# Kernel tuning notes

Measured on AMD Instinct MI355X. Metric: run time of the kernel, lower is better.

Reference implementation:

```python
import jax, jax.numpy as jnp
import numpy as np

PATCH = 3  # patch_size

def _extract_patches(feat):
    # feat: (c, h, w) -> (n_patches, c*9), patches in row-major spatial order
    c, h, w = feat.shape
    p = jax.lax.conv_general_dilated_patches(feat[None], (PATCH, PATCH), (1, 1), 'VALID')
    return p[0].reshape(c * PATCH * PATCH, -1).T  # (n, c*9)

def _match_single(feat_in, feat_ref):
    # faithful to feature_match_index(is_norm=True, norm_input=True)
    c, h, w = feat_in.shape
    def pxnorm(f):
        # F.normalize over channel dim per pixel (eps=1e-12)
        v = f.reshape(c, -1)
        n = jnp.sqrt(jnp.sum(v * v, axis=0, keepdims=True))
        return (v / jnp.maximum(n, 1e-12)).reshape(c, h, w)
    fi = pxnorm(feat_in)
    fr = pxnorm(feat_ref)
    pin = _extract_patches(fi)    # (n_in, c*9)
    pref = _extract_patches(fr)   # (n_ref, c*9)
    pref = pref / (jnp.sqrt(jnp.sum(pref * pref, axis=1, keepdims=True)) + 1e-5)
    corr = pin @ pref.T           # (n_in, n_ref) dense correlation volume
    max_idx = jnp.argmax(corr, axis=1)
    max_val = jnp.max(corr, axis=1)
    max_val = max_val / (jnp.sqrt(jnp.sum(pin * pin, axis=1)) + 1e-5)  # norm_input
    hh, ww = h - PATCH + 1, w - PATCH + 1
    return max_idx.reshape(hh, ww), max_val.reshape(hh, ww)

def _index_to_flow(max_idx):
    # max_idx: (B, hh, ww) int -> flow (B, hh+2, ww+2, 2), channels = (dx, dy)
    B, hh, ww = max_idx.shape
    fw = (max_idx % ww).astype(jnp.float32)
    fh = (max_idx // ww).astype(jnp.float32)
    gx = jnp.arange(ww, dtype=jnp.float32)[None, None, :]
    gy = jnp.arange(hh, dtype=jnp.float32)[None, :, None]
    flow = jnp.stack([fw - gx, fh - gy], axis=-1)
    return jnp.pad(flow, ((0, 0), (0, 2), (0, 2), (0, 0)))

def _shift(x, sh, sw):
    # tensor_shift with fill 0: new[:, sh:, sw:] = x[:, :h-sh, :w-sw]
    B, h, w, c = x.shape
    return jnp.pad(x, ((0, 0), (sh, 0), (sw, 0), (0, 0)))[:, :h, :w, :]

def _conv(x, w, b):
    y = jax.lax.conv_general_dilated(x, w, (1, 1), 'SAME',
                                     dimension_numbers=('NCHW', 'OIHW', 'NCHW'))
    return y + b[None, :, None, None]

def _pool(x):
    return jax.lax.reduce_window(x, -jnp.inf, jax.lax.max, (1, 1, 2, 2), (1, 1, 2, 2), 'VALID')

def _vgg(img, w11, b11, w12, b12, w21, b21, w22, b22, w31, b31):
    mean = jnp.array([0.485, 0.456, 0.406], jnp.float32).reshape(1, 3, 1, 1)
    std = jnp.array([0.229, 0.224, 0.225], jnp.float32).reshape(1, 3, 1, 1)
    x = (img - mean) / std
    x = jax.nn.relu(_conv(x, w11, b11)); relu1_1 = x
    x = jax.nn.relu(_conv(x, w12, b12))
    x = _pool(x)
    x = jax.nn.relu(_conv(x, w21, b21)); relu2_1 = x
    x = jax.nn.relu(_conv(x, w22, b22))
    x = _pool(x)
    x = jax.nn.relu(_conv(x, w31, b31)); relu3_1 = x
    return relu1_1, relu2_1, relu3_1

def setup_inputs() -> dict:
    key = jax.random.key(0)
    ks = jax.random.split(key, 8)
    B, C, H, W = 4, 256, 64, 64
    inp = {}
    inp['dense_features1'] = jax.random.normal(ks[0], (B, C, H, W), jnp.float32)
    inp['dense_features2'] = jax.random.normal(ks[1], (B, C, H, W), jnp.float32)
    inp['img_ref_hr'] = jax.random.uniform(ks[2], (B, 3, 4 * H, 4 * W), dtype=jnp.float32)
    def cw(k, o, i):
        return jax.random.normal(k, (o, i, 3, 3), jnp.float32) * np.sqrt(2.0 / (i * 9))
    inp['w11'] = cw(ks[3], 64, 3);    inp['b11'] = jnp.zeros((64,), jnp.float32)
    inp['w12'] = cw(ks[4], 64, 64);   inp['b12'] = jnp.zeros((64,), jnp.float32)
    inp['w21'] = cw(ks[5], 128, 64);  inp['b21'] = jnp.zeros((128,), jnp.float32)
    inp['w22'] = cw(ks[6], 128, 128); inp['b22'] = jnp.zeros((128,), jnp.float32)
    inp['w31'] = cw(ks[7], 256, 128); inp['b31'] = jnp.zeros((256,), jnp.float32)
    return inp

def reference(dense_features1, dense_features2, img_ref_hr,
              w11, b11, w12, b12, w21, b21, w22, b22, w31, b31):
    max_idx, max_val = jax.vmap(_match_single)(dense_features1, dense_features2)
    # relu3 scale
    sim3 = jnp.pad(max_val, ((0, 0), (1, 1), (1, 1)))[:, None]        # (B,1,h,w)
    flow3 = _index_to_flow(max_idx)                                    # (B,h,w,2)
    off3 = jnp.stack([_shift(flow3, i, j) for i in range(3) for j in range(3)], axis=1)
    # relu2 scale (x2)
    sim2 = jnp.repeat(jnp.repeat(sim3, 2, axis=2), 2, axis=3)
    flow2 = jnp.repeat(jnp.repeat(flow3, 2, axis=1), 2, axis=2) * 2.0
    off2 = jnp.stack([_shift(flow2, 2 * i, 2 * j) for i in range(3) for j in range(3)], axis=1)
    # relu1 scale (x4)
    sim1 = jnp.repeat(jnp.repeat(sim2, 2, axis=2), 2, axis=3)
    flow1 = jnp.repeat(jnp.repeat(flow3, 4, axis=1), 4, axis=2) * 4.0
    off1 = jnp.stack([_shift(flow1, 4 * i, 4 * j) for i in range(3) for j in range(3)], axis=1)
    relu1_1, relu2_1, relu3_1 = _vgg(img_ref_hr, w11, b11, w12, b12, w21, b21, w22, b22, w31, b31)
    return (off3, off2, off1, flow3, flow2, flow1, sim3, sim2, sim1, relu1_1, relu2_1, relu3_1)
```

## Files before the change

kernel.cpp:

```cpp
#include <hip/hip_runtime.h>
#include <cstdint>
#include <cstddef>

#define HW 4096
#define NPQ 3844

#define O_OFF3 0
#define O_OFF2 294912
#define O_OFF1 1474560
#define O_FLOW3 6193152
#define O_FLOW2 6225920
#define O_FLOW1 6356992
#define O_SIM3 6881280
#define O_SIM2 6897664
#define O_SIM1 6963200
#define O_R1 7225344
#define O_R2 24002560
#define O_R3 32391168

typedef __attribute__((ext_vector_type(8))) short bf16x8;
typedef __attribute__((ext_vector_type(4))) float f32x4;
typedef unsigned short ushort;
typedef unsigned int uint;

__device__ __forceinline__ ushort f2bu(float f){
  uint u = __float_as_uint(f);
  uint r = (u + 0x7fffu + ((u >> 16) & 1u)) >> 16;
  return (ushort)r;
}
__device__ __forceinline__ uint umax2x16(uint a, uint b){
  uint ah = a >> 16, bh = b >> 16, al = a & 0xffffu, bl = b & 0xffffu;
  uint h = ah > bh ? ah : bh, l = al > bl ? al : bl;
  return (h << 16) | l;
}

__device__ __forceinline__ void gll16(const float* g, float* l){
  __builtin_amdgcn_global_load_lds(
      (const __attribute__((address_space(1))) void*)g,
      (__attribute__((address_space(3))) void*)l, 16, 0, 0);
}


__global__ __launch_bounds__(256) void k_norm2(const float* __restrict__ fA,
                                               const float* __restrict__ fB,
                                               float* __restrict__ fnA,
                                               float* __restrict__ fnB,
                                               float* __restrict__ spixA,
                                               float* __restrict__ spixB,
                                               size_t inStride, size_t outStride,
                                               int sStride){
  const size_t zb = blockIdx.z;
  const float* f  = (blockIdx.y ? fB  : fA) + zb*inStride;
  float* fn       = (blockIdx.y ? fnB : fnA) + zb*outStride;
  float* spix     = (blockIdx.y ? spixB : spixA) + zb*(size_t)sStride;
  __shared__ float red[16][17];
  const int px = threadIdx.x & 15, cg = threadIdx.x >> 4;
  const int pix = blockIdx.x*16 + px;
  float v[16];
  float s = 0.f;
  #pragma unroll
  for (int i=0;i<16;i++){ v[i] = f[(cg*16+i)*HW + pix]; s += v[i]*v[i]; }
  red[cg][px] = s; __syncthreads();
  for (int off=8; off>0; off>>=1){
    if (cg < off) red[cg][px] += red[cg+off][px];
    __syncthreads();
  }
  float n = fmaxf(sqrtf(red[0][px]), 1e-12f);
  float s2 = 0.f;
  #pragma unroll
  for (int i=0;i<16;i++){
    float w = v[i] / n;
    fn[(cg*16+i)*HW + pix] = w;
    s2 += w*w;
  }
  __syncthreads();
  red[cg][px] = s2; __syncthreads();
  for (int off=8; off>0; off>>=1){
    if (cg < off) red[cg][px] += red[cg+off][px];
    __syncthreads();
  }
  if (cg == 0) spix[pix] = red[0][px];
}

__global__ __launch_bounds__(256) void k_normpq(const float* __restrict__ s1,
                                                const float* __restrict__ s2,
                                                float* __restrict__ normP,
                                                float* __restrict__ normQ,
                                                int sStride, int nStride){
  int p = blockIdx.x*256 + threadIdx.x;
  if (p >= NPQ) return;
  const size_t zb = blockIdx.z;
  s1 += zb*(size_t)sStride; s2 += zb*(size_t)sStride;
  normP += zb*(size_t)nStride; normQ += zb*(size_t)nStride;
  int py = p/62, px = p - py*62;
  float a=0.f, b=0.f;
  for (int dy=0;dy<3;dy++)
    for (int dx=0;dx<3;dx++){
      int o = (py+dy)*64 + px+dx;
      a += s1[o]; b += s2[o];
    }
  normP[p] = sqrtf(a) + 1e-5f;
  normQ[p] = sqrtf(b) + 1e-5f;
}

__global__ __launch_bounds__(256) void k_gemm(const float* __restrict__ A,
                                              const float* __restrict__ B,
                                              float* __restrict__ E,
                                              size_t abStride, size_t eStride){
  __shared__ __align__(16) float As[2][16][128];
  __shared__ __align__(16) float Bs[2][16][256];
  const size_t zb = blockIdx.z;
  A += zb*abStride; B += zb*abStride; E += zb*eStride;
  const int m0 = blockIdx.y*128, n0 = blockIdx.x*256;
  const int tid = threadIdx.x;
  const int ty = tid>>4, tx = tid&15;
  const int wave = tid>>6;

  const int arow = tid>>5;
  const int acol = (tid&31)*4;
  const int brow = tid>>6;
  const int bcol = (tid&63)*4;
  const float* Ag = A + (size_t)arow*HW + m0 + acol;
  const float* Bg = B + (size_t)brow*HW + n0 + bcol;

  float acc[8][16];
  #pragma unroll
  for (int i=0;i<8;i++)
    #pragma unroll
    for (int j=0;j<16;j++) acc[i][j]=0.f;

  {
    float* ad = &As[0][0][0] + wave*256;
    float* bd = &Bs[0][0][0] + wave*256;
    gll16(Ag,                    ad);
    gll16(Ag + (size_t)8*HW,     ad + 1024);
    gll16(Bg,                    bd);
    gll16(Bg + (size_t)4*HW,     bd + 1024);
    gll16(Bg + (size_t)8*HW,     bd + 2048);
    gll16(Bg + (size_t)12*HW,    bd + 3072);
  }
  __syncthreads();

  for (int t=0;t<16;t++){
    const int cur = t&1;
    if (t < 15){
      const float* An = Ag + (size_t)(t+1)*16*HW;
      const float* Bn = Bg + (size_t)(t+1)*16*HW;
      float* ad = &As[cur^1][0][0] + wave*256;
      float* bd = &Bs[cur^1][0][0] + wave*256;
      gll16(An,                  ad);
      gll16(An + (size_t)8*HW,   ad + 1024);
      gll16(Bn,                  bd);
      gll16(Bn + (size_t)4*HW,   bd + 1024);
      gll16(Bn + (size_t)8*HW,   bd + 2048);
      gll16(Bn + (size_t)12*HW,  bd + 3072);
    }
    #pragma unroll
    for (int k=0;k<16;k++){
      float4 a0 = *(const float4*)&As[cur][k][ty*8];
      float4 a1 = *(const float4*)&As[cur][k][ty*8+4];
      float4 b0 = *(const float4*)&Bs[cur][k][tx*4];
      float4 b1 = *(const float4*)&Bs[cur][k][64+tx*4];
      float4 b2 = *(const float4*)&Bs[cur][k][128+tx*4];
      float4 b3 = *(const float4*)&Bs[cur][k][192+tx*4];
#define GEMM_ROW(i, AV)                                   \
      acc[i][0]  = fmaf(AV, b0.x, acc[i][0]);             \
      acc[i][1]  = fmaf(AV, b0.y, acc[i][1]);             \
      acc[i][2]  = fmaf(AV, b0.z, acc[i][2]);             \
      acc[i][3]  = fmaf(AV, b0.w, acc[i][3]);             \
      acc[i][4]  = fmaf(AV, b1.x, acc[i][4]);             \
      acc[i][5]  = fmaf(AV, b1.y, acc[i][5]);             \
      acc[i][6]  = fmaf(AV, b1.z, acc[i][6]);             \
      acc[i][7]  = fmaf(AV, b1.w, acc[i][7]);             \
      acc[i][8]  = fmaf(AV, b2.x, acc[i][8]);             \
      acc[i][9]  = fmaf(AV, b2.y, acc[i][9]);             \
      acc[i][10] = fmaf(AV, b2.z, acc[i][10]);            \
      acc[i][11] = fmaf(AV, b2.w, acc[i][11]);            \
      acc[i][12] = fmaf(AV, b3.x, acc[i][12]);            \
      acc[i][13] = fmaf(AV, b3.y, acc[i][13]);            \
      acc[i][14] = fmaf(AV, b3.z, acc[i][14]);            \
      acc[i][15] = fmaf(AV, b3.w, acc[i][15]);
      GEMM_ROW(0, a0.x)
      GEMM_ROW(1, a0.y)
      GEMM_ROW(2, a0.z)
      GEMM_ROW(3, a0.w)
      GEMM_ROW(4, a1.x)
      GEMM_ROW(5, a1.y)
      GEMM_ROW(6, a1.z)
      GEMM_ROW(7, a1.w)
#undef GEMM_ROW
    }
    __syncthreads();
  }

  #pragma unroll
  for (int i=0;i<8;i++){
    float* rowp = E + (size_t)(m0+ty*8+i)*HW + n0;
    *(float4*)(rowp + tx*4)       = make_float4(acc[i][0], acc[i][1], acc[i][2], acc[i][3]);
    *(float4*)(rowp + 64 + tx*4)  = make_float4(acc[i][4], acc[i][5], acc[i][6], acc[i][7]);
    *(float4*)(rowp + 128 + tx*4) = make_float4(acc[i][8], acc[i][9], acc[i][10], acc[i][11]);
    *(float4*)(rowp + 192 + tx*4) = make_float4(acc[i][12], acc[i][13], acc[i][14], acc[i][15]);
  }
}

__global__ __launch_bounds__(256) void k_reduce(const float* __restrict__ E,
                                                const float* __restrict__ normP,
                                                const float* __restrict__ normQ,
                                                float* __restrict__ maxval,
                                                int* __restrict__ maxidx,
                                                size_t eStride, int nStride){
  const int orig = blockIdx.x;
  const int xcd = orig & 7, ii = orig >> 3;
  const int qc = NPQ >> 3, rc = NPQ & 7;
  const int p = (xcd < rc) ? xcd*(qc+1) + ii : rc*(qc+1) + (xcd-rc)*qc + ii;

  const int bz = blockIdx.y;
  E += (size_t)bz*eStride;
  normP += (size_t)bz*(size_t)nStride;
  normQ += (size_t)bz*(size_t)nStride;
  const int py = p/62, px = p - py*62;
  const int t = threadIdx.x;
  float best = -3.0e38f; int bq = 1<<30;

  if (t < 248){
    const int qy = t >> 2, g = t & 3;
    const int qx0 = g*16;
    const int cnt = (g==3) ? 14 : 16;
    float s[16];
    #pragma unroll
    for (int j=0;j<16;j++) s[j]=0.f;
    #pragma unroll
    for (int dy=0;dy<3;dy++){
      const int cbase = (qy+dy)*64 + qx0;
      #pragma unroll
      for (int dx=0;dx<3;dx++){
        const float* row = E + (size_t)((py+dy)*64 + px+dx)*HW + cbase;
        float4 w0 = *(const float4*)(row);
        float4 w1 = *(const float4*)(row+4);
        float4 w2 = *(const float4*)(row+8);
        float4 w3 = *(const float4*)(row+12);
        float4 w4 = (g<3) ? *(const float4*)(row+16) : make_float4(0.f,0.f,0.f,0.f);
        float w[20] = {w0.x,w0.y,w0.z,w0.w, w1.x,w1.y,w1.z,w1.w,
                       w2.x,w2.y,w2.z,w2.w, w3.x,w3.y,w3.z,w3.w,
                       w4.x,w4.y,w4.z,w4.w};
        #pragma unroll
        for (int j=0;j<16;j++) s[j] += w[dx+j];
      }
    }
    const int qbase = qy*62 + qx0;
    for (int j=0;j<cnt;j++){
      float v = s[j] / normQ[qbase + j];
      if (v > best){ best = v; bq = qbase + j; }
    }
  }

  #pragma unroll
  for (int off=32; off>0; off>>=1){
    float ov = __shfl_xor(best, off);
    int   oi = __shfl_xor(bq, off);
    if (ov > best || (ov == best && oi < bq)){ best = ov; bq = oi; }
  }
  __shared__ float wv[4];
  __shared__ int   wi[4];
  if ((t & 63) == 0){ wv[t>>6] = best; wi[t>>6] = bq; }
  __syncthreads();
  if (t == 0){
    float v = wv[0]; int bi = wi[0];
    #pragma unroll
    for (int w2=1; w2<4; w2++){
      float ov = wv[w2]; int oi = wi[w2];
      if (ov > v || (ov == v && oi < bi)){ v = ov; bi = oi; }
    }
    maxval[bz*NPQ + p] = v / normP[p];
    maxidx[bz*NPQ + p] = bi;
  }
}


__global__ __launch_bounds__(256) void k_flow3(const int* __restrict__ maxidx,
                                               const float* __restrict__ maxval,
                                               float* __restrict__ flow3ws,
                                               float* __restrict__ sim3ws,
                                               float* __restrict__ oflow,
                                               float* __restrict__ osim){
  int idx = blockIdx.x*256 + threadIdx.x;
  if (idx >= 4*HW) return;
  int b = idx >> 12, r = idx & 4095;
  int y = r >> 6, x = r & 63;
  float fx = 0.f, fy = 0.f;
  if (y < 62 && x < 62){
    int mi = maxidx[b*NPQ + y*62 + x];
    int qy = mi/62, qx = mi - qy*62;
    fx = (float)(qx - x);
    fy = (float)(qy - y);
  }
  flow3ws[idx*2] = fx; flow3ws[idx*2+1] = fy;
  oflow[idx*2] = fx; oflow[idx*2+1] = fy;
  float sv = 0.f;
  if (y >= 1 && y <= 62 && x >= 1 && x <= 62)
    sv = maxval[b*NPQ + (y-1)*62 + (x-1)];
  sim3ws[idx] = sv;
  osim[idx] = sv;
}

__global__ __launch_bounds__(256) void k_outs(const float* __restrict__ fl3,
                                              const float* __restrict__ sm3,
                                              float* __restrict__ out){
  int idx = blockIdx.x*256 + threadIdx.x;

  if (idx < 147456){
    int b = idx / 36864;
    int rem = idx - b*36864;
    int k = rem >> 12;
    int r = rem & 4095;
    int y = r >> 6, x = r & 63;
    int i = k/3, j = k - i*3;
    float fx = 0.f, fy = 0.f;
    if (y >= i && x >= j){
      int s = (b*HW + (y-i)*64 + (x-j))*2;
      fx = fl3[s]; fy = fl3[s+1];
    }
    out[O_OFF3 + (size_t)idx*2] = fx; out[O_OFF3 + (size_t)idx*2+1] = fy;
    return;
  }
  idx -= 147456;
  if (idx < 589824){
    int b = idx / 147456;
    int rem = idx - b*147456;
    int k = rem / 16384;
    int r = rem - k*16384;
    int y = r >> 7, x = r & 127;
    int i = k/3, j = k - i*3;
    float fx = 0.f, fy = 0.f;
    int sy = y - 2*i, sx = x - 2*j;
    if (sy >= 0 && sx >= 0){
      int s = (b*HW + (sy/2)*64 + (sx/2))*2;
      fx = fl3[s] * 2.f; fy = fl3[s+1] * 2.f;
    }
    out[O_OFF2 + (size_t)idx*2] = fx; out[O_OFF2 + (size_t)idx*2+1] = fy;
    return;
  }
  idx -= 589824;
  if (idx < 2359296){
    int b = idx / 589824;
    int rem = idx - b*589824;
    int k = rem / 65536;
    int r = rem - k*65536;
    int y = r >> 8, x = r & 255;
    int i = k/3, j = k - i*3;
    float fx = 0.f, fy = 0.f;
    int sy = y - 4*i, sx = x - 4*j;
    if (sy >= 0 && sx >= 0){
      int s = (b*HW + (sy/4)*64 + (sx/4))*2;
      fx = fl3[s] * 4.f; fy = fl3[s+1] * 4.f;
    }
    out[O_OFF1 + (size_t)idx*2] = fx; out[O_OFF1 + (size_t)idx*2+1] = fy;
    return;
  }
  idx -= 2359296;
  if (idx < 65536){
    int b = idx / 16384;
    int r = idx - b*16384;
    int y = r >> 7, x = r & 127;
    int s = b*HW + (y/2)*64 + (x/2);
    out[O_FLOW2 + (size_t)idx*2]   = fl3[s*2]   * 2.f;
    out[O_FLOW2 + (size_t)idx*2+1] = fl3[s*2+1] * 2.f;
    return;
  }
  idx -= 65536;
  if (idx < 262144){
    int b = idx / 65536;
    int r = idx - b*65536;
    int y = r >> 8, x = r & 255;
    int s = b*HW + (y/4)*64 + (x/4);
    out[O_FLOW1 + (size_t)idx*2]   = fl3[s*2]   * 4.f;
    out[O_FLOW1 + (size_t)idx*2+1] = fl3[s*2+1] * 4.f;
    return;
  }
  idx -= 262144;
  if (idx < 65536){
    int b = idx / 16384;
    int r = idx - b*16384;
    int y = r >> 7, x = r & 127;
    int s = b*HW + (y/2)*64 + (x/2);
    out[O_SIM2 + (size_t)idx] = sm3[s];
    return;
  }
  idx -= 65536;
  if (idx < 262144){
    int b = idx / 65536;
    int r = idx - b*65536;
    int y = r >> 8, x = r & 255;
    int s = b*HW + (y/4)*64 + (x/4);
    out[O_SIM1 + (size_t)idx] = sm3[s];
  }
}


__global__ __launch_bounds__(256) void k_wt(const float* __restrict__ w,
                                            ushort* __restrict__ wt,
                                            int Cout, int Cin){
  int idx = blockIdx.x*256 + threadIdx.x;
  int tot = Cout*Cin*9;
  if (idx >= tot) return;
  int o = idx / (Cin*9);
  int rem = idx - o*(Cin*9);
  int i = rem / 9;
  int tap = rem - i*9;
  wt[((size_t)tap*Cout + o)*Cin + i] = f2bu(w[idx]);
}

__global__ __launch_bounds__(256) void k_conv1(const float* __restrict__ img,
                                               const float* __restrict__ w,
                                               const float* __restrict__ bias,
                                               float* __restrict__ outf,
                                               ushort* __restrict__ outb){
  __shared__ float sIn[3][18][20];
  __shared__ float sW[8][3][9];
  const int tx = threadIdx.x & 15, ty = threadIdx.x >> 4;
  const int x0 = blockIdx.x*16, y0 = blockIdx.y*16;
  const int b = blockIdx.z >> 3;
  const int oc0 = (blockIdx.z & 7)*8;
  const float MEAN[3] = {0.485f,0.456f,0.406f};
  const float STDV[3] = {0.229f,0.224f,0.225f};
  const float* in = img + (size_t)b*3*65536;
  for (int i = threadIdx.x; i < 3*324; i += 256){
    int ci = i / 324;
    int rr = i - ci*324;
    int iy = rr / 18, ix = rr - iy*18;
    int gy = y0 + iy - 1, gx = x0 + ix - 1;
    float v = 0.f;
    if (gy >= 0 && gy < 256 && gx >= 0 && gx < 256)
      v = (in[ci*65536 + gy*256 + gx] - MEAN[ci]) / STDV[ci];
    sIn[ci][iy][ix] = v;
  }
  if (threadIdx.x < 216){
    int o = threadIdx.x / 27;
    int rr = threadIdx.x - o*27;
    int ci = rr / 9, t = rr - ci*9;
    sW[o][ci][t] = w[((oc0+o)*3 + ci)*9 + t];
  }
  __syncthreads();
  float acc[8] = {0.f,0.f,0.f,0.f,0.f,0.f,0.f,0.f};
  for (int ci=0; ci<3; ci++){
    #pragma unroll
    for (int ky=0;ky<3;ky++){
      #pragma unroll
      for (int kx=0;kx<3;kx++){
        float v = sIn[ci][ty+ky][tx+kx];
        #pragma unroll
        for (int o=0;o<8;o++)
          acc[o] = fmaf(v, sW[o][ci][ky*3+kx], acc[o]);
      }
    }
  }
  #pragma unroll
  for (int o=0;o<8;o++){
    float r = fmaxf(acc[o] + bias[oc0+o], 0.f);
    outf[(size_t)b*4194304 + (size_t)(oc0+o)*65536 + (size_t)(y0+ty)*256 + (x0+tx)] = r;
    outb[(size_t)b*4194304 + ((size_t)(y0+ty)*256 + (x0+tx))*64 + (oc0+o)] = f2bu(r);
  }
}

__global__ __launch_bounds__(256) void k_conv_mfma(const ushort* __restrict__ X,
                                                   const ushort* __restrict__ Wt,
                                                   const float* __restrict__ bias,
                                                   ushort* __restrict__ outHWC,
                                                   float* __restrict__ outCHW,
                                                   int Cin, int Cout, int H, int W,
                                                   int zDiv, size_t xStride,
                                                   size_t hwcStride, size_t chwStride){
  extern __shared__ ushort smem[];
  const int CS = Cin + 8;
  ushort* sX = smem;
  const int tid = threadIdx.x;
  const int wave = tid >> 6, lane = tid & 63;
  const int quad = lane >> 4, l16 = lane & 15;
  const int bz = blockIdx.z / zDiv;
  const int zo = blockIdx.z - bz*zDiv;
  const int x0 = blockIdx.x * 16, y0 = blockIdx.y * 8, oc0 = zo * 64;
  X += (size_t)bz * xStride;
  if (outHWC) outHWC += (size_t)bz * hwcStride;
  if (outCHW) outCHW += (size_t)bz * chwStride;
  const int nci8 = Cin >> 3;
  const int c8s = (Cin == 128) ? 4 : 3;
  const int c8m = nci8 - 1;

  for (int i = tid; i < 180*nci8; i += 256){
    int c8 = i & c8m;
    int rest = i >> c8s;
    int px = rest % 18;
    int row = rest / 18;
    int gy = y0 - 1 + row, gx = x0 - 1 + px;
    uint4 v = make_uint4(0u,0u,0u,0u);
    if (gy >= 0 && gy < H && gx >= 0 && gx < W)
      v = *(const uint4*)(X + ((size_t)gy*W + gx)*Cin + c8*8);
    *(uint4*)(sX + (row*18 + px)*CS + c8*8) = v;
  }
  __syncthreads();

  f32x4 acc[2][4];
  #pragma unroll
  for (int m=0;m<2;m++)
    #pragma unroll
    for (int r=0;r<4;r++) acc[m][r] = (f32x4){0.f,0.f,0.f,0.f};

  const int my = (wave>>1)*4;
  const int mo = (wave&1)*32;

  for (int tap = 0; tap < 9; tap++){
    int dy = tap/3 - 1, dx = tap - (tap/3)*3 - 1;
    const ushort* wsrc = Wt + ((size_t)tap*Cout + oc0)*Cin;
    for (int k0 = 0; k0 < Cin; k0 += 32){
      bf16x8 A0 = *(const bf16x8*)(wsrc + (mo + l16)*Cin + k0 + quad*8);
      bf16x8 A1 = *(const bf16x8*)(wsrc + (mo + 16 + l16)*Cin + k0 + quad*8);
      #pragma unroll
      for (int r = 0; r < 4; r++){
        bf16x8 B = *(const bf16x8*)(sX + ((1 + my + r + dy)*18 + (1 + l16 + dx))*CS + k0 + quad*8);
        acc[0][r] = __builtin_amdgcn_mfma_f32_16x16x32_bf16(A0, B, acc[0][r], 0, 0, 0);
        acc[1][r] = __builtin_amdgcn_mfma_f32_16x16x32_bf16(A1, B, acc[1][r], 0, 0, 0);
      }
    }
  }

  const int x = x0 + l16;
  #pragma unroll
  for (int m = 0; m < 2; m++){
    int ocb = oc0 + mo + m*16 + quad*4;
    float4 bv = *(const float4*)(bias + ocb);
    #pragma unroll
    for (int r = 0; r < 4; r++){
      int y = y0 + my + r;
      float v0 = fmaxf(acc[m][r][0] + bv.x, 0.f);
      float v1 = fmaxf(acc[m][r][1] + bv.y, 0.f);
      float v2 = fmaxf(acc[m][r][2] + bv.z, 0.f);
      float v3 = fmaxf(acc[m][r][3] + bv.w, 0.f);
      if (outHWC){
        uint lo = (uint)f2bu(v0) | ((uint)f2bu(v1) << 16);
        uint hi = (uint)f2bu(v2) | ((uint)f2bu(v3) << 16);
        uint2* dst = (uint2*)(outHWC + ((size_t)y*W + x)*Cout + ocb);
        *dst = make_uint2(lo, hi);
      }
      if (outCHW){
        size_t base = (size_t)ocb*H*W + (size_t)y*W + x;
        outCHW[base]                 = v0;
        outCHW[base +   (size_t)H*W] = v1;
        outCHW[base + 2*(size_t)H*W] = v2;
        outCHW[base + 3*(size_t)H*W] = v3;
      }
    }
  }
}

__global__ __launch_bounds__(256) void k_pool_h(const ushort* __restrict__ in,
                                                ushort* __restrict__ out,
                                                int C, int Wo, int s,
                                                size_t inStride, size_t outStride){
  in  += (size_t)blockIdx.z * inStride;
  out += (size_t)blockIdx.z * outStride;
  int idx = blockIdx.x*256 + threadIdx.x;
  int nc8 = C >> 3;
  if (idx >= Wo*nc8) return;
  int x = idx >> s;
  int c8 = idx & (nc8 - 1);
  int y = blockIdx.y;
  int Wi = 2*Wo;
  const ushort* p = in + ((size_t)(2*y)*Wi + 2*x)*C + c8*8;
  uint4 a = *(const uint4*)p;
  uint4 b = *(const uint4*)(p + C);
  uint4 c = *(const uint4*)(p + (size_t)Wi*C);
  uint4 d = *(const uint4*)(p + (size_t)Wi*C + C);
  uint4 m;
  m.x = umax2x16(umax2x16(a.x,b.x), umax2x16(c.x,d.x));
  m.y = umax2x16(umax2x16(a.y,b.y), umax2x16(c.y,d.y));
  m.z = umax2x16(umax2x16(a.z,b.z), umax2x16(c.z,d.z));
  m.w = umax2x16(umax2x16(a.w,b.w), umax2x16(c.w,d.w));
  *(uint4*)(out + ((size_t)y*Wo + x)*C + c8*8) = m;
}


extern "C" void kernel_launch(void* const* d_in, const int* in_sizes, int n_in,
                              void* d_out, int out_size, void* d_ws, size_t ws_size,
                              hipStream_t stream){
  const float* f1  = (const float*)d_in[0];
  const float* f2  = (const float*)d_in[1];
  const float* img = (const float*)d_in[2];
  const float* w11 = (const float*)d_in[3];  const float* b11 = (const float*)d_in[4];
  const float* w12 = (const float*)d_in[5];  const float* b12 = (const float*)d_in[6];
  const float* w21 = (const float*)d_in[7];  const float* b21 = (const float*)d_in[8];
  const float* w22 = (const float*)d_in[9];  const float* b22 = (const float*)d_in[10];
  const float* w31 = (const float*)d_in[11]; const float* b31 = (const float*)d_in[12];
  float* out = (float*)d_out;

  float* F = (float*)d_ws;
  float* E = F;

  ushort* wt1  = (ushort*)(F + 16777216);
  ushort* wt2a = (ushort*)(F + 16795648);
  ushort* wt2b = (ushort*)(F + 16832512);
  ushort* wt3  = (ushort*)(F + 16906240);

  ushort* EU  = (ushort*)E;
  ushort* t1a = EU;
  ushort* t2a = EU + 16777216;
  ushort* p1a = EU;
  ushort* t3a = EU + 4194304;
  ushort* t4a = EU + 16777216;
  ushort* p2a = EU;

  const bool big = ws_size >= 302600000ull;

  float *mval, *fl3, *sm3; int* midx;

  if (big){
    float* f1n = F + 67108864;
    float* f2n = F + 71303168;
    float* s1  = F + 75497472;
    float* s2  = F + 75513856;
    float* nP  = F + 75530240;
    float* nQ  = F + 75546624;
    mval = F + 75563008;
    midx = (int*)(F + 75579392);
    fl3  = F + 75595776;
    sm3  = F + 75628544;

    k_norm2<<<dim3(256,2,4),256,0,stream>>>(f1, f2, f1n, f2n, s1, s2,
                                            (size_t)256*HW, 1048576, 4096);
    k_normpq<<<dim3(16,1,4),256,0,stream>>>(s1, s2, nP, nQ, 4096, 4096);
    k_gemm<<<dim3(16,32,4),256,0,stream>>>(f1n, f2n, E, 1048576, 16777216);
    k_reduce<<<dim3(NPQ,4),256,0,stream>>>(E, nP, nQ, mval, midx, 16777216, 4096);
  } else {
    float* f1n  = F + 16777216;
    float* f2n  = F + 17825792;
    float* s1   = F + 18874368;
    float* s2   = F + 18878464;
    float* nP   = F + 18882560;
    float* nQ   = F + 18886656;
    mval = F + 18890752;
    midx = (int*)(F + 18907136);
    fl3  = F + 18923520;
    sm3  = F + 18956288;

    for (int b=0;b<4;b++){
      const float* f1b  = f1 + (size_t)b*256*HW;
      const float* f2b2 = f2 + (size_t)b*256*HW;
      k_norm2<<<dim3(256,2,1),256,0,stream>>>(f1b, f2b2, f1n, f2n, s1, s2, 0, 0, 0);
      k_normpq<<<dim3(16,1,1),256,0,stream>>>(s1, s2, nP, nQ, 0, 0);
      k_gemm<<<dim3(16,32,1),256,0,stream>>>(f1n, f2n, E, 0, 0);
      k_reduce<<<dim3(NPQ,1),256,0,stream>>>(E, nP, nQ, mval + b*NPQ, midx + b*NPQ, 0, 0);
    }
  }

  k_flow3<<<64,256,0,stream>>>(midx, mval, fl3, sm3, out+O_FLOW3, out+O_SIM3);
  k_outs<<<14656,256,0,stream>>>(fl3, sm3, out);

  k_wt<<<144,256,0,stream>>>(w12, wt1, 64, 64);
  k_wt<<<288,256,0,stream>>>(w21, wt2a, 128, 64);
  k_wt<<<576,256,0,stream>>>(w22, wt2b, 128, 128);
  k_wt<<<1152,256,0,stream>>>(w31, wt3, 256, 128);

  const int smem64  = 180*72*2;
  const int smem128 = 180*136*2;

  k_conv1<<<dim3(16,16,32),256,0,stream>>>(img, w11, b11, out + O_R1, t1a);
  k_conv_mfma<<<dim3(16,32,4),256,smem64,stream>>>(t1a, wt1, b12, t2a, nullptr,
      64, 64, 256, 256, 1, 4194304, 4194304, 0);
  k_pool_h<<<dim3(4,128,4),256,0,stream>>>(t2a, p1a, 64, 128, 3, 4194304, 1048576);
  k_conv_mfma<<<dim3(8,16,8),256,smem64,stream>>>(p1a, wt2a, b21, t3a, out + O_R2,
      64, 128, 128, 128, 2, 1048576, 2097152, 2097152);
  k_conv_mfma<<<dim3(8,16,8),256,smem128,stream>>>(t3a, wt2b, b22, t4a, nullptr,
      128, 128, 128, 128, 2, 2097152, 2097152, 0);
  k_pool_h<<<dim3(4,64,4),256,0,stream>>>(t4a, p2a, 128, 64, 4, 2097152, 524288);
  k_conv_mfma<<<dim3(4,8,16),256,smem128,stream>>>(p2a, wt3, b31, nullptr, out + O_R3,
      128, 256, 64, 64, 4, 524288, 0, 1048576);
}
```

Measured before the change: 1.017 ms.

## Compute four adjacent patch reductions per block, fuse weight transposes, pack conv1 stores

The correlation reduce kernel now handles four horizontally adjacent input patches per block. Each row of E it loads is reused across overlapping 3x3 windows, so a block reads 6 rows instead of 3 per patch, and the grid shrinks from 3844 to 992 blocks. The four weight-transpose launches are merged into one kernel, and conv1 writes its eight bf16 HWC outputs as one 16-byte store instead of eight scalar stores. The reduce change raises register pressure (4x16 accumulators per thread) and may lower occupancy.

```diff
diff --git a/kernel.cpp b/kernel.cpp
--- a/kernel.cpp
+++ b/kernel.cpp
@@ -203,74 +203,102 @@
   }
 }
 
-__global__ __launch_bounds__(256) void k_reduce(const float* __restrict__ E,
-                                                const float* __restrict__ normP,
-                                                const float* __restrict__ normQ,
-                                                float* __restrict__ maxval,
-                                                int* __restrict__ maxidx,
-                                                size_t eStride, int nStride){
+__global__ __launch_bounds__(256) void k_reduce4(const float* __restrict__ E,
+                                                 const float* __restrict__ normP,
+                                                 const float* __restrict__ normQ,
+                                                 float* __restrict__ maxval,
+                                                 int* __restrict__ maxidx,
+                                                 size_t eStride, int nStride){
   const int orig = blockIdx.x;
-  const int xcd = orig & 7, ii = orig >> 3;
-  const int qc = NPQ >> 3, rc = NPQ & 7;
-  const int p = (xcd < rc) ? xcd*(qc+1) + ii : rc*(qc+1) + (xcd-rc)*qc + ii;
+  const int blk = (orig & 7)*124 + (orig >> 3);
+  const int py = blk >> 4, pxg = blk & 15;
+  const int px0 = pxg*4;
+  const int U = (px0 == 60) ? 2 : 4;
 
   const int bz = blockIdx.y;
   E += (size_t)bz*eStride;
   normP += (size_t)bz*(size_t)nStride;
   normQ += (size_t)bz*(size_t)nStride;
-  const int py = p/62, px = p - py*62;
   const int t = threadIdx.x;
-  float best = -3.0e38f; int bq = 1<<30;
+
+  float best[4]; int bq[4];
+  #pragma unroll
+  for (int u=0;u<4;u++){ best[u] = -3.0e38f; bq[u] = 1<<30; }
 
   if (t < 248){
     const int qy = t >> 2, g = t & 3;
     const int qx0 = g*16;
     const int cnt = (g==3) ? 14 : 16;
-    float s[16];
-    #pragma unroll
-    for (int j=0;j<16;j++) s[j]=0.f;
+    float s[4][16];
+    #pragma unroll
+    for (int u=0;u<4;u++)
+      #pragma unroll
+      for (int j=0;j<16;j++) s[u][j]=0.f;
+
     #pragma unroll
     for (int dy=0;dy<3;dy++){
       const int cbase = (qy+dy)*64 + qx0;
+      const float* rowbase = E + (size_t)((py+dy)*64 + px0)*HW + cbase;
       #pragma unroll
-      for (int dx=0;dx<3;dx++){
-        const float* row = E + (size_t)((py+dy)*64 + px+dx)*HW + cbase;
-        float4 w0 = *(const float4*)(row);
-        float4 w1 = *(const float4*)(row+4);
-        float4 w2 = *(const float4*)(row+8);
-        float4 w3 = *(const float4*)(row+12);
-        float4 w4 = (g<3) ? *(const float4*)(row+16) : make_float4(0.f,0.f,0.f,0.f);
-        float w[20] = {w0.x,w0.y,w0.z,w0.w, w1.x,w1.y,w1.z,w1.w,
-                       w2.x,w2.y,w2.z,w2.w, w3.x,w3.y,w3.z,w3.w,
-                       w4.x,w4.y,w4.z,w4.w};
-        #pragma unroll
-        for (int j=0;j<16;j++) s[j] += w[dx+j];
+      for (int c=0;c<6;c++){
+        if (c < U+2){
+          const float* row = rowbase + (size_t)c*HW;
+          float4 w0 = *(const float4*)(row);
+          float4 w1 = *(const float4*)(row+4);
+          float4 w2 = *(const float4*)(row+8);
+          float4 w3 = *(const float4*)(row+12);
+          float4 w4 = (g<3) ? *(const float4*)(row+16) : make_float4(0.f,0.f,0.f,0.f);
+          float w[20] = {w0.x,w0.y,w0.z,w0.w, w1.x,w1.y,w1.z,w1.w,
+                         w2.x,w2.y,w2.z,w2.w, w3.x,w3.y,w3.z,w3.w,
+                         w4.x,w4.y,w4.z,w4.w};
+          #pragma unroll
+          for (int u=0;u<4;u++){
+            const int dx = c - u;
+            if (dx >= 0 && dx <= 2){
+              #pragma unroll
+              for (int j=0;j<16;j++) s[u][j] += w[dx+j];
+            }
+          }
+        }
       }
     }
     const int qbase = qy*62 + qx0;
-    for (int j=0;j<cnt;j++){
-      float v = s[j] / normQ[qbase + j];
-      if (v > best){ best = v; bq = qbase + j; }
-    }
-  }
-
-  #pragma unroll
-  for (int off=32; off>0; off>>=1){
-    float ov = __shfl_xor(best, off);
-    int   oi = __shfl_xor(bq, off);
-    if (ov > best || (ov == best && oi < bq)){ best = ov; bq = oi; }
-  }
-  __shared__ float wv[4];
-  __shared__ int   wi[4];
-  if ((t & 63) == 0){ wv[t>>6] = best; wi[t>>6] = bq; }
+    #pragma unroll
+    for (int u=0;u<4;u++){
+      if (u < U){
+        for (int j=0;j<cnt;j++){
+          float v = s[u][j] / normQ[qbase + j];
+          if (v > best[u]){ best[u] = v; bq[u] = qbase + j; }
+        }
+      }
+    }
+  }
+
+  #pragma unroll
+  for (int u=0;u<4;u++){
+    #pragma unroll
+    for (int off=32; off>0; off>>=1){
+      float ov = __shfl_xor(best[u], off);
+      int   oi = __shfl_xor(bq[u], off);
+      if (ov > best[u] || (ov == best[u] && oi < bq[u])){ best[u] = ov; bq[u] = oi; }
+    }
+  }
+  __shared__ float wv[4][4];
+  __shared__ int   wi[4][4];
+  if ((t & 63) == 0){
+    const int wv_w = t>>6;
+    #pragma unroll
+    for (int u=0;u<4;u++){ wv[wv_w][u] = best[u]; wi[wv_w][u] = bq[u]; }
+  }
   __syncthreads();
-  if (t == 0){
-    float v = wv[0]; int bi = wi[0];
+  if (t < U){
+    float v = wv[0][t]; int bi = wi[0][t];
     #pragma unroll
     for (int w2=1; w2<4; w2++){
-      float ov = wv[w2]; int oi = wi[w2];
+      float ov = wv[w2][t]; int oi = wi[w2][t];
       if (ov > v || (ov == v && oi < bi)){ v = ov; bi = oi; }
     }
+    const int p = py*62 + px0 + t;
     maxval[bz*NPQ + p] = v / normP[p];
     maxidx[bz*NPQ + p] = bi;
   }
@@ -397,17 +425,26 @@
 }
 
 
-__global__ __launch_bounds__(256) void k_wt(const float* __restrict__ w,
-                                            ushort* __restrict__ wt,
-                                            int Cout, int Cin){
+__global__ __launch_bounds__(256) void k_wt4(const float* __restrict__ w12,
+                                             const float* __restrict__ w21,
+                                             const float* __restrict__ w22,
+                                             const float* __restrict__ w31,
+                                             ushort* __restrict__ wt1,
+                                             ushort* __restrict__ wt2a,
+                                             ushort* __restrict__ wt2b,
+                                             ushort* __restrict__ wt3){
   int idx = blockIdx.x*256 + threadIdx.x;
-  int tot = Cout*Cin*9;
-  if (idx >= tot) return;
+  const float* w; ushort* wt; int Cin, Cout;
+  if (idx < 36864){ w=w12; wt=wt1; Cin=64; Cout=64; }
+  else if (idx < 110592){ idx-=36864;  w=w21; wt=wt2a; Cin=64;  Cout=128; }
+  else if (idx < 258048){ idx-=110592; w=w22; wt=wt2b; Cin=128; Cout=128; }
+  else if (idx < 552960){ idx-=258048; w=w31; wt=wt3;  Cin=128; Cout=256; }
+  else return;
   int o = idx / (Cin*9);
   int rem = idx - o*(Cin*9);
   int i = rem / 9;
   int tap = rem - i*9;
-  wt[((size_t)tap*Cout + o)*Cin + i] = f2bu(w[idx]);
+  wt[((size_t)tap*Cout + o)*Cin + i] = f2bu(w[(size_t)(o*Cin + i)*9 + tap]);
 }
 
 __global__ __launch_bounds__(256) void k_conv1(const float* __restrict__ img,
@@ -454,12 +491,19 @@
       }
     }
   }
+  float r8[8];
   #pragma unroll
   for (int o=0;o<8;o++){
     float r = fmaxf(acc[o] + bias[oc0+o], 0.f);
+    r8[o] = r;
     outf[(size_t)b*4194304 + (size_t)(oc0+o)*65536 + (size_t)(y0+ty)*256 + (x0+tx)] = r;
-    outb[(size_t)b*4194304 + ((size_t)(y0+ty)*256 + (x0+tx))*64 + (oc0+o)] = f2bu(r);
-  }
+  }
+  uint4 pk;
+  pk.x = (uint)f2bu(r8[0]) | ((uint)f2bu(r8[1]) << 16);
+  pk.y = (uint)f2bu(r8[2]) | ((uint)f2bu(r8[3]) << 16);
+  pk.z = (uint)f2bu(r8[4]) | ((uint)f2bu(r8[5]) << 16);
+  pk.w = (uint)f2bu(r8[6]) | ((uint)f2bu(r8[7]) << 16);
+  *(uint4*)(outb + (size_t)b*4194304 + ((size_t)(y0+ty)*256 + (x0+tx))*64 + oc0) = pk;
 }
 
 __global__ __launch_bounds__(256) void k_conv_mfma(const ushort* __restrict__ X,
@@ -628,7 +672,7 @@
                                             (size_t)256*HW, 1048576, 4096);
     k_normpq<<<dim3(16,1,4),256,0,stream>>>(s1, s2, nP, nQ, 4096, 4096);
     k_gemm<<<dim3(16,32,4),256,0,stream>>>(f1n, f2n, E, 1048576, 16777216);
-    k_reduce<<<dim3(NPQ,4),256,0,stream>>>(E, nP, nQ, mval, midx, 16777216, 4096);
+    k_reduce4<<<dim3(992,4),256,0,stream>>>(E, nP, nQ, mval, midx, 16777216, 4096);
   } else {
     float* f1n  = F + 16777216;
     float* f2n  = F + 17825792;
@@ -647,17 +691,14 @@
       k_norm2<<<dim3(256,2,1),256,0,stream>>>(f1b, f2b2, f1n, f2n, s1, s2, 0, 0, 0);
       k_normpq<<<dim3(16,1,1),256,0,stream>>>(s1, s2, nP, nQ, 0, 0);
       k_gemm<<<dim3(16,32,1),256,0,stream>>>(f1n, f2n, E, 0, 0);
-      k_reduce<<<dim3(NPQ,1),256,0,stream>>>(E, nP, nQ, mval + b*NPQ, midx + b*NPQ, 0, 0);
+      k_reduce4<<<dim3(992,1),256,0,stream>>>(E, nP, nQ, mval + b*NPQ, midx + b*NPQ, 0, 0);
     }
   }
 
   k_flow3<<<64,256,0,stream>>>(midx, mval, fl3, sm3, out+O_FLOW3, out+O_SIM3);
   k_outs<<<14656,256,0,stream>>>(fl3, sm3, out);
 
-  k_wt<<<144,256,0,stream>>>(w12, wt1, 64, 64);
-  k_wt<<<288,256,0,stream>>>(w21, wt2a, 128, 64);
-  k_wt<<<576,256,0,stream>>>(w22, wt2b, 128, 128);
-  k_wt<<<1152,256,0,stream>>>(w31, wt3, 256, 128);
+  k_wt4<<<2160,256,0,stream>>>(w12, w21, w22, w31, wt1, wt2a, wt2b, wt3);
 
   const int smem64  = 180*72*2;
   const int smem128 = 180*136*2;
```

Result: slower. 1.482 ms (+45.6%).
